# Kernel tuning notes

Hardware: AMD Instinct MI355X
Metric: run time of the kernel (lower is better)

## Reference

```python
import jax, jax.numpy as jnp
import numpy as np

B, L, H, HKV, D, E = 2, 2048, 8, 1, 256, 2048
SCALING = D ** -0.5


def rotate_half(x):
    x1, x2 = jnp.split(x, 2, axis=-1)
    return jnp.concatenate([-x2, x1], axis=-1)


def setup_inputs() -> dict:
    key = jax.random.key(0)
    ks = jax.random.split(key, 5)
    hidden_states = jax.random.normal(ks[0], (B, L, E), jnp.float32)
    attention_mask = jnp.zeros((B, 1, 1, L, L), jnp.float32)  # additive mask (all visible)
    # standard RoPE tables, shape [L, D]
    inv_freq = 1.0 / (10000.0 ** (jnp.arange(0, D, 2, dtype=jnp.float32) / D))
    freqs = jnp.arange(L, dtype=jnp.float32)[:, None] * inv_freq[None, :]
    emb = jnp.concatenate([freqs, freqs], axis=-1)
    cos, sin = jnp.cos(emb), jnp.sin(emb)
    s = 0.02
    Wq = jax.random.normal(ks[1], (H * D, E), jnp.float32) * s
    Wk = jax.random.normal(ks[2], (HKV * D, E), jnp.float32) * s
    Wv = jax.random.normal(ks[3], (HKV * D, E), jnp.float32) * s
    Wo = jax.random.normal(ks[4], (E, H * D), jnp.float32) * s
    return {"hidden_states": hidden_states, "attention_mask": attention_mask,
            "cos": cos, "sin": sin, "Wq": Wq, "Wk": Wk, "Wv": Wv, "Wo": Wo}


def reference(hidden_states, attention_mask, cos, sin, Wq, Wk, Wv, Wo):
    b, l, _ = hidden_states.shape
    q = jnp.einsum('ble,de->bld', hidden_states, Wq)
    k = jnp.einsum('ble,de->bld', hidden_states, Wk)
    v = jnp.einsum('ble,de->bld', hidden_states, Wv)
    # q: [B, L, 1, H, D] -> transpose(1,3) -> [B, H, 1, L, D]
    q = jnp.transpose(q.reshape(b, l, 1, H, D), (0, 3, 2, 1, 4))
    # k, v: [B, 1, L, Hkv, D] -> transpose(2,3) -> [B, 1, Hkv, L, D]
    k = jnp.transpose(k.reshape(b, 1, l, HKV, D), (0, 1, 3, 2, 4))
    v = jnp.transpose(v.reshape(b, 1, l, HKV, D), (0, 1, 3, 2, 4))
    # RoPE (cos/sin broadcast over leading dims)
    q = q * cos + rotate_half(q) * sin
    k = k * cos + rotate_half(k) * sin
    # scores: [B, H, Hkv, L, L]
    attn = jnp.matmul(q, jnp.swapaxes(k, -1, -2)) * SCALING
    attn = attn + attention_mask
    attn = jax.nn.softmax(attn.astype(jnp.float32), axis=-1)
    out = jnp.matmul(attn, v)                         # [B, H, Hkv, L, D]
    out = jnp.transpose(out, (0, 1, 3, 2, 4))         # [B, H, L, Hkv, D]
    out = out.reshape(b, l, H * D)                    # row-major reshape, as torch .reshape
    return jnp.einsum('bld,ed->ble', out, Wo)
```

## Files before the change

### kernel.cpp

```cpp
#include <hip/hip_runtime.h>

typedef unsigned short u16;
typedef __attribute__((ext_vector_type(8))) short short8;
typedef __attribute__((ext_vector_type(4))) float f32x4;

struct __align__(8) US4 { u16 x, y, z, w; };

__device__ __forceinline__ u16 f2bf(float x) {
  union { float f; unsigned u; } c; c.f = x;
  unsigned r = c.u + 0x7fffu + ((c.u >> 16) & 1u);
  return (u16)(r >> 16);
}
__device__ __forceinline__ float bf2f(u16 u) {
  union { unsigned u; float f; } c; c.u = ((unsigned)u) << 16;
  return c.f;
}
__device__ __forceinline__ void gload_lds16(const void* g, void* l) {
  __builtin_amdgcn_global_load_lds(
      (const __attribute__((address_space(1))) void*)g,
      (__attribute__((address_space(3))) void*)l, 16, 0, 0);
}
__device__ __forceinline__ f32x4 fzero4() {
  f32x4 z; z[0] = 0.f; z[1] = 0.f; z[2] = 0.f; z[3] = 0.f; return z;
}

__global__ __launch_bounds__(256) void cvt_kernel(const float* __restrict__ src,
                                                  u16* __restrict__ dst, int n) {
  int i = (blockIdx.x * 256 + threadIdx.x) * 4;
  if (i + 3 < n) {
    float4 v = *(const float4*)(src + i);
    US4 o = { f2bf(v.x), f2bf(v.y), f2bf(v.z), f2bf(v.w) };
    *(US4*)(dst + i) = o;
  }
}

template <int MODE>
__global__ __launch_bounds__(256) void gemm_nt(
    const u16* __restrict__ A, const u16* __restrict__ Bw,
    u16* __restrict__ q_out, u16* __restrict__ k_out, u16* __restrict__ v_out,
    float* __restrict__ c_out) {
  __shared__ u16 lA[128 * 32];
  __shared__ u16 lB[128 * 32];
  const int K = 2048;
  int t = threadIdx.x, w = t >> 6, lane = t & 63;
  int wm = w >> 1, wn = w & 1;
  int m0 = blockIdx.x * 128, n0 = blockIdx.y * 128;
  int g = lane >> 4, qi = lane & 15;

  f32x4 acc[4][4];
#pragma unroll
  for (int i = 0; i < 4; i++)
#pragma unroll
    for (int j = 0; j < 4; j++) acc[i][j] = fzero4();

  for (int k0 = 0; k0 < K; k0 += 32) {
#pragma unroll
    for (int i = 0; i < 2; i++) {
      int off = i * 4096 + w * 1024 + lane * 16;
      int row = off >> 6, cg = (off >> 4) & 3;
      gload_lds16(A + (size_t)(m0 + row) * K + k0 + cg * 8,
                  (char*)lA + i * 4096 + w * 1024);
      gload_lds16(Bw + (size_t)(n0 + row) * K + k0 + cg * 8,
                  (char*)lB + i * 4096 + w * 1024);
    }
    __syncthreads();
    short8 af[4], bfr[4];
#pragma unroll
    for (int f = 0; f < 4; f++) {
      int ra = wm * 64 + f * 16 + qi;
      int rb = wn * 64 + f * 16 + qi;
      int kb2 = g * 16;
      af[f] = *(const short8*)((const char*)lA + ra * 64 + kb2);
      bfr[f] = *(const short8*)((const char*)lB + rb * 64 + kb2);
    }
#pragma unroll
    for (int i = 0; i < 4; i++)
#pragma unroll
      for (int j = 0; j < 4; j++)
        acc[i][j] = __builtin_amdgcn_mfma_f32_16x16x32_bf16(af[i], bfr[j], acc[i][j], 0, 0, 0);
    __syncthreads();
  }

#pragma unroll
  for (int i = 0; i < 4; i++) {
#pragma unroll
    for (int j = 0; j < 4; j++) {
#pragma unroll
      for (int r = 0; r < 4; r++) {
        int m = m0 + wm * 64 + i * 16 + g * 4 + r;
        int n = n0 + wn * 64 + j * 16 + qi;
        float v = acc[i][j][r];
        if (MODE == 0) {
          int b = m >> 11, l = m & 2047;
          if (n < 2048) {
            int h = n >> 8, d = n & 255;
            q_out[(((size_t)(b * 8 + h) * 2048) + l) * 256 + d] = f2bf(v);
          } else if (n < 2304) {
            int d = n - 2048;
            k_out[((size_t)b * 2048 + l) * 256 + d] = f2bf(v);
          } else {
            int d = n - 2304;
            v_out[((size_t)b * 256 + d) * 2048 + l] = f2bf(v);
          }
        } else {
          c_out[(size_t)m * 2048 + n] = v;
        }
      }
    }
  }
}

__global__ __launch_bounds__(256) void rope_kernel(u16* __restrict__ q, u16* __restrict__ k,
                                                   const float* __restrict__ cosT,
                                                   const float* __restrict__ sinT) {
  int idx = blockIdx.x * 2 + (threadIdx.x >> 7);
  int d = threadIdx.x & 127;
  u16* ptr;
  int l;
  float sc;
  if (idx < 32768) { ptr = q + (size_t)idx * 256; l = idx & 2047; sc = 0.0625f; }
  else             { ptr = k + (size_t)(idx - 32768) * 256; l = (idx - 32768) & 2047; sc = 1.0f; }
  float x1 = bf2f(ptr[d]), x2 = bf2f(ptr[d + 128]);
  float c1 = cosT[l * 256 + d], s1 = sinT[l * 256 + d];
  float c2 = cosT[l * 256 + d + 128], s2 = sinT[l * 256 + d + 128];
  float o1 = (x1 * c1 - x2 * s1) * sc;
  float o2 = (x2 * c2 + x1 * s2) * sc;
  ptr[d] = f2bf(o1);
  ptr[d + 128] = f2bf(o2);
}

__global__ __launch_bounds__(256, 2) void flash_kernel(
    const u16* __restrict__ qr, const u16* __restrict__ kr,
    const u16* __restrict__ vt_g, u16* __restrict__ attnout) {
  __shared__ u16 kt[64 * 256];
  __shared__ u16 vt[256 * 64];
  __shared__ u16 pl[4][16 * 64];

  int t = threadIdx.x, w = t >> 6, lane = t & 63;
  int qi = lane & 15, g = lane >> 4;
  int b = blockIdx.z, h = blockIdx.y;
  int l0 = blockIdx.x * 64 + w * 16;

  short8 qf[8];
  const u16* qbase = qr + ((size_t)((b * 8 + h) * 2048) + l0 + qi) * 256 + g * 8;
#pragma unroll
  for (int ks = 0; ks < 8; ks++) qf[ks] = *(const short8*)(qbase + ks * 32);

  f32x4 ot[16];
#pragma unroll
  for (int fd = 0; fd < 16; fd++) ot[fd] = fzero4();
  float mrow = -1e30f, lrow = 0.f;

  const u16* kb = kr + (size_t)b * (2048 * 256);
  const u16* vb = vt_g + (size_t)b * (256 * 2048);

  for (int kv = 0; kv < 2048; kv += 64) {
#pragma unroll
    for (int i = 0; i < 8; i++) {
      int off = i * 4096 + w * 1024 + lane * 16;
      int row = off >> 9, gc = (off >> 4) & 31;
      int gs = gc ^ (row & 7);
      gload_lds16(kb + (size_t)(kv + row) * 256 + gs * 8, (char*)kt + i * 4096 + w * 1024);
    }
#pragma unroll
    for (int i = 0; i < 8; i++) {
      int off = i * 4096 + w * 1024 + lane * 16;
      int d = off >> 7, gc = (off >> 4) & 7;
      int gs = gc ^ (d & 7);
      gload_lds16(vb + (size_t)d * 2048 + kv + gs * 8, (char*)vt + i * 4096 + w * 1024);
    }
    __syncthreads();

    f32x4 st[4];
#pragma unroll
    for (int f = 0; f < 4; f++) {
      st[f] = fzero4();
      int row = f * 16 + qi;
#pragma unroll
      for (int ks = 0; ks < 8; ks++) {
        int slot = (4 * ks + g) ^ (row & 7);
        short8 kf = *(const short8*)((const char*)kt + row * 512 + slot * 16);
        st[f] = __builtin_amdgcn_mfma_f32_16x16x32_bf16(kf, qf[ks], st[f], 0, 0, 0);
      }
    }

    float tmax = -1e30f;
#pragma unroll
    for (int f = 0; f < 4; f++)
#pragma unroll
      for (int r = 0; r < 4; r++) tmax = fmaxf(tmax, st[f][r]);
    tmax = fmaxf(tmax, __shfl_xor(tmax, 16));
    tmax = fmaxf(tmax, __shfl_xor(tmax, 32));
    float mnew = fmaxf(mrow, tmax);
    float scale = __expf(mrow - mnew);
    float tsum = 0.f;
#pragma unroll
    for (int f = 0; f < 4; f++)
#pragma unroll
      for (int r = 0; r < 4; r++) {
        float p = __expf(st[f][r] - mnew);
        st[f][r] = p;
        tsum += p;
      }
    tsum += __shfl_xor(tsum, 16);
    tsum += __shfl_xor(tsum, 32);
    lrow = lrow * scale + tsum;
    mrow = mnew;
#pragma unroll
    for (int fd = 0; fd < 16; fd++)
#pragma unroll
      for (int r = 0; r < 4; r++) ot[fd][r] *= scale;

#pragma unroll
    for (int f = 0; f < 4; f++) {
      US4 pw = { f2bf(st[f][0]), f2bf(st[f][1]), f2bf(st[f][2]), f2bf(st[f][3]) };
      int byte_ = (qi * 128 + f * 32 + g * 8) ^ ((qi & 7) << 4);
      *(US4*)((char*)pl[w] + byte_) = pw;
    }

#pragma unroll
    for (int s = 0; s < 2; s++) {
      int pb_ = (qi * 128 + s * 64 + g * 16) ^ ((qi & 7) << 4);
      short8 pf = *(const short8*)((const char*)pl[w] + pb_);
#pragma unroll
      for (int fd = 0; fd < 16; fd++) {
        int d = fd * 16 + qi;
        int slot = (s * 4 + g) ^ (d & 7);
        short8 vf = *(const short8*)((const char*)vt + d * 128 + slot * 16);
        ot[fd] = __builtin_amdgcn_mfma_f32_16x16x32_bf16(vf, pf, ot[fd], 0, 0, 0);
      }
    }
    __syncthreads();
  }

  float inv = 1.f / lrow;
  u16* ob = attnout + ((size_t)((b * 8 + h) * 2048) + l0 + qi) * 256;
#pragma unroll
  for (int fd = 0; fd < 16; fd++) {
    US4 o = { f2bf(ot[fd][0] * inv), f2bf(ot[fd][1] * inv),
              f2bf(ot[fd][2] * inv), f2bf(ot[fd][3] * inv) };
    *(US4*)(ob + fd * 16 + g * 4) = o;
  }
}

extern "C" void kernel_launch(void* const* d_in, const int* in_sizes, int n_in,
                              void* d_out, int out_size, void* d_ws, size_t ws_size,
                              hipStream_t stream) {
  const float* hidden = (const float*)d_in[0];
  const float* cosT = (const float*)d_in[2];
  const float* sinT = (const float*)d_in[3];
  const float* Wq = (const float*)d_in[4];
  const float* Wk = (const float*)d_in[5];
  const float* Wv = (const float*)d_in[6];
  const float* Wo = (const float*)d_in[7];

  char* ws = (char*)d_ws;
  u16* Xbf  = (u16*)(ws + 0);
  u16* Wqkv = (u16*)(ws + 16777216);
  u16* Wob  = (u16*)(ws + 27262976);
  u16* qbuf = (u16*)(ws + 35651584);
  u16* kbuf = (u16*)(ws + 52428800);
  u16* vT   = (u16*)(ws + 54525952);
  u16* attn = (u16*)(ws + 56623104);
  float* out = (float*)d_out;

  cvt_kernel<<<8192, 256, 0, stream>>>(hidden, Xbf, 8388608);
  cvt_kernel<<<4096, 256, 0, stream>>>(Wq, Wqkv, 4194304);
  cvt_kernel<<<512, 256, 0, stream>>>(Wk, Wqkv + 4194304, 524288);
  cvt_kernel<<<512, 256, 0, stream>>>(Wv, Wqkv + 4718592, 524288);
  cvt_kernel<<<4096, 256, 0, stream>>>(Wo, Wob, 4194304);

  gemm_nt<0><<<dim3(32, 20), 256, 0, stream>>>(Xbf, Wqkv, qbuf, kbuf, vT, nullptr);
  rope_kernel<<<18432, 256, 0, stream>>>(qbuf, kbuf, cosT, sinT);
  flash_kernel<<<dim3(32, 8, 2), 256, 0, stream>>>(qbuf, kbuf, vT, attn);
  gemm_nt<1><<<dim3(32, 16), 256, 0, stream>>>(attn, Wob, nullptr, nullptr, nullptr, out);
}
```

Measured before the change: 265.1 us.

## Double-buffer K/V, process two query groups per wave, merge conversion kernels

```diff
diff --git a/kernel.cpp b/kernel.cpp
--- a/kernel.cpp
+++ b/kernel.cpp
@@ -24,14 +24,22 @@
   f32x4 z; z[0] = 0.f; z[1] = 0.f; z[2] = 0.f; z[3] = 0.f; return z;
 }
 
-__global__ __launch_bounds__(256) void cvt_kernel(const float* __restrict__ src,
-                                                  u16* __restrict__ dst, int n) {
-  int i = (blockIdx.x * 256 + threadIdx.x) * 4;
-  if (i + 3 < n) {
-    float4 v = *(const float4*)(src + i);
-    US4 o = { f2bf(v.x), f2bf(v.y), f2bf(v.z), f2bf(v.w) };
-    *(US4*)(dst + i) = o;
-  }
+__global__ __launch_bounds__(256) void cvt_all(
+    const float* __restrict__ h, const float* __restrict__ wq,
+    const float* __restrict__ wk, const float* __restrict__ wv,
+    const float* __restrict__ wo, u16* __restrict__ Xbf,
+    u16* __restrict__ Wqkv, u16* __restrict__ Wob) {
+  int b = blockIdx.x;
+  const float* s; u16* d; int off;
+  if (b < 8192)       { s = h;  d = Xbf;            off = b; }
+  else if (b < 12288) { s = wq; d = Wqkv;           off = b - 8192; }
+  else if (b < 12800) { s = wk; d = Wqkv + 4194304; off = b - 12288; }
+  else if (b < 13312) { s = wv; d = Wqkv + 4718592; off = b - 12800; }
+  else                { s = wo; d = Wob;            off = b - 13312; }
+  int i = (off * 256 + threadIdx.x) * 4;
+  float4 v = *(const float4*)(s + i);
+  US4 o = { f2bf(v.x), f2bf(v.y), f2bf(v.z), f2bf(v.w) };
+  *(US4*)(d + i) = o;
 }
 
 template <int MODE>
@@ -93,14 +101,14 @@
         if (MODE == 0) {
           int b = m >> 11, l = m & 2047;
           if (n < 2048) {
-            int h = n >> 8, d = n & 255;
-            q_out[(((size_t)(b * 8 + h) * 2048) + l) * 256 + d] = f2bf(v);
+            int h = n >> 8, dd = n & 255;
+            q_out[(((size_t)(b * 8 + h) * 2048) + l) * 256 + dd] = f2bf(v);
           } else if (n < 2304) {
-            int d = n - 2048;
-            k_out[((size_t)b * 2048 + l) * 256 + d] = f2bf(v);
+            int dd = n - 2048;
+            k_out[((size_t)b * 2048 + l) * 256 + dd] = f2bf(v);
           } else {
-            int d = n - 2304;
-            v_out[((size_t)b * 256 + d) * 2048 + l] = f2bf(v);
+            int dd = n - 2304;
+            v_out[((size_t)b * 256 + dd) * 2048 + l] = f2bf(v);
           }
         } else {
           c_out[(size_t)m * 2048 + n] = v;
@@ -129,117 +137,144 @@
   ptr[d + 128] = f2bf(o2);
 }
 
-__global__ __launch_bounds__(256, 2) void flash_kernel(
+__global__ __launch_bounds__(256, 1) void flash_kernel(
     const u16* __restrict__ qr, const u16* __restrict__ kr,
     const u16* __restrict__ vt_g, u16* __restrict__ attnout) {
-  __shared__ u16 kt[64 * 256];
-  __shared__ u16 vt[256 * 64];
-  __shared__ u16 pl[4][16 * 64];
+  __shared__ u16 kt[2][64 * 256];
+  __shared__ u16 vt[2][256 * 64];
+  __shared__ u16 pl[4][2048];
 
   int t = threadIdx.x, w = t >> 6, lane = t & 63;
   int qi = lane & 15, g = lane >> 4;
   int b = blockIdx.z, h = blockIdx.y;
-  int l0 = blockIdx.x * 64 + w * 16;
-
-  short8 qf[8];
-  const u16* qbase = qr + ((size_t)((b * 8 + h) * 2048) + l0 + qi) * 256 + g * 8;
-#pragma unroll
-  for (int ks = 0; ks < 8; ks++) qf[ks] = *(const short8*)(qbase + ks * 32);
-
-  f32x4 ot[16];
-#pragma unroll
-  for (int fd = 0; fd < 16; fd++) ot[fd] = fzero4();
-  float mrow = -1e30f, lrow = 0.f;
+  int bh = b * 8 + h;
+  int l0 = blockIdx.x * 128 + w * 32;
 
   const u16* kb = kr + (size_t)b * (2048 * 256);
   const u16* vb = vt_g + (size_t)b * (256 * 2048);
 
-  for (int kv = 0; kv < 2048; kv += 64) {
+  short8 qf[2][8];
+#pragma unroll
+  for (int qg = 0; qg < 2; qg++) {
+    const u16* qbase = qr + ((size_t)bh * 2048 + l0 + qg * 16 + qi) * 256 + g * 8;
+#pragma unroll
+    for (int ks = 0; ks < 8; ks++) qf[qg][ks] = *(const short8*)(qbase + ks * 32);
+  }
+
+  f32x4 ot[16][2];
+#pragma unroll
+  for (int fd = 0; fd < 16; fd++) { ot[fd][0] = fzero4(); ot[fd][1] = fzero4(); }
+  float mrow[2] = { -1e30f, -1e30f }, lrow[2] = { 0.f, 0.f };
+
+  auto stage = [&](int buf, int kv) {
 #pragma unroll
     for (int i = 0; i < 8; i++) {
       int off = i * 4096 + w * 1024 + lane * 16;
       int row = off >> 9, gc = (off >> 4) & 31;
       int gs = gc ^ (row & 7);
-      gload_lds16(kb + (size_t)(kv + row) * 256 + gs * 8, (char*)kt + i * 4096 + w * 1024);
+      gload_lds16(kb + (size_t)(kv + row) * 256 + gs * 8,
+                  (char*)kt[buf] + i * 4096 + w * 1024);
     }
 #pragma unroll
     for (int i = 0; i < 8; i++) {
       int off = i * 4096 + w * 1024 + lane * 16;
       int d = off >> 7, gc = (off >> 4) & 7;
       int gs = gc ^ (d & 7);
-      gload_lds16(vb + (size_t)d * 2048 + kv + gs * 8, (char*)vt + i * 4096 + w * 1024);
-    }
-    __syncthreads();
-
-    f32x4 st[4];
+      gload_lds16(vb + (size_t)d * 2048 + kv + gs * 8,
+                  (char*)vt[buf] + i * 4096 + w * 1024);
+    }
+  };
+
+  stage(0, 0);
+  __syncthreads();
+
+  for (int tt = 0; tt < 32; ++tt) {
+    int cur = tt & 1;
+    if (tt < 31) stage(cur ^ 1, (tt + 1) * 64);
+
+    f32x4 st[4][2];
+    const char* kbase = (const char*)kt[cur];
 #pragma unroll
     for (int f = 0; f < 4; f++) {
-      st[f] = fzero4();
+      st[f][0] = fzero4(); st[f][1] = fzero4();
       int row = f * 16 + qi;
 #pragma unroll
       for (int ks = 0; ks < 8; ks++) {
         int slot = (4 * ks + g) ^ (row & 7);
-        short8 kf = *(const short8*)((const char*)kt + row * 512 + slot * 16);
-        st[f] = __builtin_amdgcn_mfma_f32_16x16x32_bf16(kf, qf[ks], st[f], 0, 0, 0);
+        short8 kf = *(const short8*)(kbase + row * 512 + slot * 16);
+        st[f][0] = __builtin_amdgcn_mfma_f32_16x16x32_bf16(kf, qf[0][ks], st[f][0], 0, 0, 0);
+        st[f][1] = __builtin_amdgcn_mfma_f32_16x16x32_bf16(kf, qf[1][ks], st[f][1], 0, 0, 0);
       }
     }
 
-    float tmax = -1e30f;
-#pragma unroll
-    for (int f = 0; f < 4; f++)
-#pragma unroll
-      for (int r = 0; r < 4; r++) tmax = fmaxf(tmax, st[f][r]);
-    tmax = fmaxf(tmax, __shfl_xor(tmax, 16));
-    tmax = fmaxf(tmax, __shfl_xor(tmax, 32));
-    float mnew = fmaxf(mrow, tmax);
-    float scale = __expf(mrow - mnew);
-    float tsum = 0.f;
-#pragma unroll
-    for (int f = 0; f < 4; f++)
-#pragma unroll
-      for (int r = 0; r < 4; r++) {
-        float p = __expf(st[f][r] - mnew);
-        st[f][r] = p;
-        tsum += p;
+#pragma unroll
+    for (int qg = 0; qg < 2; qg++) {
+      float tmax = -1e30f;
+#pragma unroll
+      for (int f = 0; f < 4; f++)
+#pragma unroll
+        for (int r = 0; r < 4; r++) tmax = fmaxf(tmax, st[f][qg][r]);
+      tmax = fmaxf(tmax, __shfl_xor(tmax, 16));
+      tmax = fmaxf(tmax, __shfl_xor(tmax, 32));
+      float mnew = fmaxf(mrow[qg], tmax);
+      float scale = __expf(mrow[qg] - mnew);
+      float tsum = 0.f;
+#pragma unroll
+      for (int f = 0; f < 4; f++)
+#pragma unroll
+        for (int r = 0; r < 4; r++) {
+          float p = __expf(st[f][qg][r] - mnew);
+          st[f][qg][r] = p;
+          tsum += p;
+        }
+      tsum += __shfl_xor(tsum, 16);
+      tsum += __shfl_xor(tsum, 32);
+      lrow[qg] = lrow[qg] * scale + tsum;
+      mrow[qg] = mnew;
+#pragma unroll
+      for (int fd = 0; fd < 16; fd++)
+#pragma unroll
+        for (int r = 0; r < 4; r++) ot[fd][qg][r] *= scale;
+
+      int qrow = qg * 16 + qi;
+#pragma unroll
+      for (int f = 0; f < 4; f++) {
+        US4 pw = { f2bf(st[f][qg][0]), f2bf(st[f][qg][1]),
+                   f2bf(st[f][qg][2]), f2bf(st[f][qg][3]) };
+        int byte_ = (qrow * 128 + f * 32 + g * 8) ^ ((qi & 7) << 4);
+        *(US4*)((char*)pl[w] + byte_) = pw;
       }
-    tsum += __shfl_xor(tsum, 16);
-    tsum += __shfl_xor(tsum, 32);
-    lrow = lrow * scale + tsum;
-    mrow = mnew;
-#pragma unroll
-    for (int fd = 0; fd < 16; fd++)
-#pragma unroll
-      for (int r = 0; r < 4; r++) ot[fd][r] *= scale;
-
-#pragma unroll
-    for (int f = 0; f < 4; f++) {
-      US4 pw = { f2bf(st[f][0]), f2bf(st[f][1]), f2bf(st[f][2]), f2bf(st[f][3]) };
-      int byte_ = (qi * 128 + f * 32 + g * 8) ^ ((qi & 7) << 4);
-      *(US4*)((char*)pl[w] + byte_) = pw;
-    }
-
+    }
+
+    const char* vbase = (const char*)vt[cur];
 #pragma unroll
     for (int s = 0; s < 2; s++) {
-      int pb_ = (qi * 128 + s * 64 + g * 16) ^ ((qi & 7) << 4);
-      short8 pf = *(const short8*)((const char*)pl[w] + pb_);
+      int pb0 = ((0 * 16 + qi) * 128 + s * 64 + g * 16) ^ ((qi & 7) << 4);
+      int pb1 = ((1 * 16 + qi) * 128 + s * 64 + g * 16) ^ ((qi & 7) << 4);
+      short8 pf0 = *(const short8*)((const char*)pl[w] + pb0);
+      short8 pf1 = *(const short8*)((const char*)pl[w] + pb1);
 #pragma unroll
       for (int fd = 0; fd < 16; fd++) {
         int d = fd * 16 + qi;
         int slot = (s * 4 + g) ^ (d & 7);
-        short8 vf = *(const short8*)((const char*)vt + d * 128 + slot * 16);
-        ot[fd] = __builtin_amdgcn_mfma_f32_16x16x32_bf16(vf, pf, ot[fd], 0, 0, 0);
+        short8 vf = *(const short8*)(vbase + d * 128 + slot * 16);
+        ot[fd][0] = __builtin_amdgcn_mfma_f32_16x16x32_bf16(vf, pf0, ot[fd][0], 0, 0, 0);
+        ot[fd][1] = __builtin_amdgcn_mfma_f32_16x16x32_bf16(vf, pf1, ot[fd][1], 0, 0, 0);
       }
     }
     __syncthreads();
   }
 
-  float inv = 1.f / lrow;
-  u16* ob = attnout + ((size_t)((b * 8 + h) * 2048) + l0 + qi) * 256;
-#pragma unroll
-  for (int fd = 0; fd < 16; fd++) {
-    US4 o = { f2bf(ot[fd][0] * inv), f2bf(ot[fd][1] * inv),
-              f2bf(ot[fd][2] * inv), f2bf(ot[fd][3] * inv) };
-    *(US4*)(ob + fd * 16 + g * 4) = o;
+#pragma unroll
+  for (int qg = 0; qg < 2; qg++) {
+    float inv = 1.f / lrow[qg];
+    u16* ob = attnout + ((size_t)bh * 2048 + l0 + qg * 16 + qi) * 256;
+#pragma unroll
+    for (int fd = 0; fd < 16; fd++) {
+      US4 o = { f2bf(ot[fd][qg][0] * inv), f2bf(ot[fd][qg][1] * inv),
+                f2bf(ot[fd][qg][2] * inv), f2bf(ot[fd][qg][3] * inv) };
+      *(US4*)(ob + fd * 16 + g * 4) = o;
+    }
   }
 }
 
@@ -264,14 +299,9 @@
   u16* attn = (u16*)(ws + 56623104);
   float* out = (float*)d_out;
 
-  cvt_kernel<<<8192, 256, 0, stream>>>(hidden, Xbf, 8388608);
-  cvt_kernel<<<4096, 256, 0, stream>>>(Wq, Wqkv, 4194304);
-  cvt_kernel<<<512, 256, 0, stream>>>(Wk, Wqkv + 4194304, 524288);
-  cvt_kernel<<<512, 256, 0, stream>>>(Wv, Wqkv + 4718592, 524288);
-  cvt_kernel<<<4096, 256, 0, stream>>>(Wo, Wob, 4194304);
-
+  cvt_all<<<17408, 256, 0, stream>>>(hidden, Wq, Wk, Wv, Wo, Xbf, Wqkv, Wob);
   gemm_nt<0><<<dim3(32, 20), 256, 0, stream>>>(Xbf, Wqkv, qbuf, kbuf, vT, nullptr);
   rope_kernel<<<18432, 256, 0, stream>>>(qbuf, kbuf, cosT, sinT);
-  flash_kernel<<<dim3(32, 8, 2), 256, 0, stream>>>(qbuf, kbuf, vT, attn);
+  flash_kernel<<<dim3(16, 8, 2), 256, 0, stream>>>(qbuf, kbuf, vT, attn);
   gemm_nt<1><<<dim3(32, 16), 256, 0, stream>>>(attn, Wob, nullptr, nullptr, nullptr, out);
 }
```

Result: slower. 300.1 us (+13.2%).
